# Optimization experiments

Measured on AMD Instinct MI355X. Metric: run time of the kernel, lower is better.

## Reference

```python
import jax, jax.numpy as jnp
import numpy as np

N = 8192      # points
NOBJ = 8      # objects
H = 64        # hidden_size (required by channel arithmetic, see notes)
CDIM = 128
K = 20
KNN = 360
EPS = 1e-5


def _lrelu(x):
    return jnp.where(x >= 0, x, 0.2 * x)


def _inorm2d(x):  # x: [C, N, K]; InstanceNorm2d, affine=False, biased var
    m = x.mean(axis=(1, 2), keepdims=True)
    v = ((x - m) ** 2).mean(axis=(1, 2), keepdims=True)
    return (x - m) / jnp.sqrt(v + EPS)


def _inorm1d(x):  # x: [C, L]
    m = x.mean(axis=1, keepdims=True)
    v = ((x - m) ** 2).mean(axis=1, keepdims=True)
    return (x - m) / jnp.sqrt(v + EPS)


def _block2d(W, f):  # 1x1 conv (no bias) + InstanceNorm2d + LeakyReLU(0.2)
    return _lrelu(_inorm2d(jnp.einsum('oc,cnk->onk', W, f)))


def _block1d(W, f):
    return _lrelu(_inorm1d(W @ f))


def _edge_feat(xc, idx):  # xc: [C, N], idx: [N, k] -> [2C, N, k]
    xt = xc.T                                   # [N, C]
    nb = xt[idx]                                # [N, k, C] gather
    ctr = jnp.broadcast_to(xt[:, None, :], nb.shape)
    return jnp.concatenate([nb - ctr, ctr], axis=2).transpose(2, 0, 1)


def _knn_idx(x, tag, k):  # kNN within same node_tag, self excluded
    xs = jax.lax.stop_gradient(x)
    sq = jnp.sum(xs * xs, axis=1)
    d2 = sq[:, None] + sq[None, :] - 2.0 * (xs @ xs.T)
    valid = (tag[:, None] == tag[None, :]) & ~jnp.eye(xs.shape[0], dtype=bool)
    d2 = jnp.where(valid, d2, jnp.inf)
    _, idx = jax.lax.top_k(-d2, k)              # ascending distance order
    return idx


def setup_inputs() -> dict:
    key = jax.random.key(0)
    ks = jax.random.split(key, 16)
    x = jax.random.normal(ks[0], (N, 3), dtype=jnp.float32)
    node_tag = (jnp.arange(N, dtype=jnp.int32) // (N // NOBJ))  # equal groups

    def w(k, o, i):
        return jax.random.normal(k, (o, i), dtype=jnp.float32) * (1.0 / np.sqrt(i))

    return {
        'x': x, 'node_tag': node_tag, 'n_obj': NOBJ,
        'W1': w(ks[1], H, 6),       'W2': w(ks[2], H, H),
        'W3': w(ks[3], H, 2 * H),   'W4': w(ks[4], H, H),
        'W5': w(ks[5], H, 2 * H),   'W6': w(ks[6], H, H),
        'W7': w(ks[7], H, 2 * H),   'W8': w(ks[8], H, H),
        'W9': w(ks[9], 128, 4 * H),
        'W10': w(ks[10], 2 * H, 3 * H),
        'W11': w(ks[11], 2 * H, 3 * H),
        'W12': w(ks[12], H, 3 * H),
        'W13': w(ks[13], H, 2 * H),
        'Wr': w(ks[14], CDIM, H),
    }


def reference(x, node_tag, n_obj, W1, W2, W3, W4, W5, W6, W7, W8, W9, W10,
              W11, W12, W13, Wr):
    n = x.shape[0]
    idx = _knn_idx(x, node_tag, KNN)            # [N, 360]

    f = _edge_feat(x.T, idx[:, :K])             # [6, N, 20]
    x1 = _block2d(W2, _block2d(W1, f)).max(axis=-1)            # [H, N]
    f = _edge_feat(x1, idx[:, :40:2])
    x2 = _block2d(W4, _block2d(W3, f)).max(axis=-1) + x1
    f = _edge_feat(x2, idx[:, :120:6])
    x3 = _block2d(W6, _block2d(W5, f)).max(axis=-1) + x2
    f = _edge_feat(x3, idx[:, :360:18])
    x4 = _block2d(W8, _block2d(W7, f)).max(axis=-1) + x3

    g = _block1d(W9, jnp.concatenate([x1, x2, x3, x4], axis=0))  # [128, N]
    g = jnp.broadcast_to(g.max(axis=1, keepdims=True), (128, n))

    x4 = _block1d(W10, jnp.concatenate([g, x4], axis=0))   # [2H, N]
    x3 = _block1d(W11, jnp.concatenate([x4, x3], axis=0))  # [2H, N]
    x2 = _block1d(W12, jnp.concatenate([x3, x2], axis=0))  # [H, N]
    x1 = _block1d(W13, jnp.concatenate([x2, x1], axis=0))  # [H, N]

    code = (Wr @ x1).T                                     # [N, c_dim]
    tag = node_tag.astype(jnp.int32)
    sums = jax.ops.segment_sum(code, tag, num_segments=n_obj)
    cnt = jax.ops.segment_sum(jnp.ones((n,), code.dtype), tag,
                              num_segments=n_obj)
    return sums / jnp.maximum(cnt, 1.0)[:, None]           # [n_obj, c_dim]
```

## Files before the change

### kernel.cpp

```cpp
#include <hip/hip_runtime.h>
#include <hip/hip_bf16.h>
#include <stdint.h>

typedef __hip_bfloat16 bf16;

#define NPTS 8192
#define KSEL 20
#define MBIG (NPTS*KSEL)
#define EPSN 1e-5f

__device__ __forceinline__ float lrelu(float x){ return x >= 0.f ? x : 0.2f*x; }
__device__ __forceinline__ float ldx(const void* p, int i, int isbf){
  return isbf ? __bfloat162float(((const bf16*)p)[i]) : ((const float*)p)[i];
}
__device__ __forceinline__ unsigned fenc(float x){
  unsigned u = __float_as_uint(x);
  return (u & 0x80000000u) ? ~u : (u | 0x80000000u);
}
__device__ __forceinline__ float fdec(unsigned u){
  return __uint_as_float((u & 0x80000000u) ? (u & 0x7FFFFFFFu) : ~u);
}
__device__ __forceinline__ unsigned long long u64min(unsigned long long a, unsigned long long b){ return a<b?a:b; }
__device__ __forceinline__ unsigned long long u64max(unsigned long long a, unsigned long long b){ return a<b?b:a; }
__device__ __forceinline__ void ce(unsigned long long &a, unsigned long long &b, bool asc){
  unsigned long long mn = a<b?a:b, mx = a<b?b:a;
  a = asc ? mn : mx;
  b = asc ? mx : mn;
}

__global__ void zero_kernel(float* __restrict__ p, int n){
  int i = blockIdx.x*256 + threadIdx.x;
  if (i < n) p[i] = 0.f;
}

__global__ void detect_kernel(const void* __restrict__ x, int* __restrict__ badf){
  int i = blockIdx.x*256 + threadIdx.x;
  int bad = 0;
  for (; i < NPTS*3; i += gridDim.x*256){
    float v = __bfloat162float(((const bf16*)x)[i]);
    if (!(fabsf(v) < 1000.0f)) bad = 1;
  }
  if (__any(bad) && (threadIdx.x & 63) == 0) atomicOr(badf, 1);
}

__global__ __launch_bounds__(256) void knn_kernel(const void* __restrict__ x,
                                                  const int* __restrict__ tag,
                                                  int* __restrict__ idxc,
                                                  const int* __restrict__ flagp){
  __shared__ unsigned long long keysL[1024];
  const int isbf = (*flagp == 0);
  const int i = blockIdx.x;
  const int base = (i >> 10) << 10;
  const int t = threadIdx.x;
  const float xi = ldx(x, i*3+0, isbf);
  const float yi = ldx(x, i*3+1, isbf);
  const float zi = ldx(x, i*3+2, isbf);
  const float sqi = xi*xi + yi*yi + zi*zi;
  const int tagi = tag[i];

  unsigned long long v[4];
  #pragma unroll
  for (int r = 0; r < 4; r++){
    int j = 4*t + r, gj = base + j;
    float xj = ldx(x, gj*3+0, isbf);
    float yj = ldx(x, gj*3+1, isbf);
    float zj = ldx(x, gj*3+2, isbf);
    float sqj = xj*xj + yj*yj + zj*zj;
    float dot = xi*xj + yi*yj + zi*zj;
    float d2 = sqi + sqj - 2.0f*dot;
    bool valid = (gj != i) && (tag[gj] == tagi);
    unsigned k = valid ? fenc(d2) : 0xFFFFFFFFu;
    v[r] = ((unsigned long long)k << 32) | (unsigned)gj;
  }

  #pragma unroll
  for (int ksz = 2; ksz <= 1024; ksz <<= 1){
    #pragma unroll
    for (int jj = ksz >> 1; jj > 0; jj >>= 1){
      if (jj >= 256){
        __syncthreads();
        keysL[4*t+0] = v[0]; keysL[4*t+1] = v[1];
        keysL[4*t+2] = v[2]; keysL[4*t+3] = v[3];
        __syncthreads();
        const int pt = t ^ (jj >> 2);
        const bool keep_min = (((t & (ksz >> 2)) == 0) == ((t & (jj >> 2)) == 0));
        #pragma unroll
        for (int r = 0; r < 4; r++){
          unsigned long long o = keysL[4*pt + r];
          v[r] = keep_min ? u64min(v[r], o) : u64max(v[r], o);
        }
      } else if (jj >= 4){
        const int mask = jj >> 2;
        const bool keep_min = (((t & (ksz >> 2)) == 0) == ((t & mask) == 0));
        #pragma unroll
        for (int r = 0; r < 4; r++){
          unsigned long long o = __shfl_xor(v[r], mask, 64);
          v[r] = keep_min ? u64min(v[r], o) : u64max(v[r], o);
        }
      } else if (jj == 2){
        const bool asc = ((t & (ksz >> 2)) == 0);
        ce(v[0], v[2], asc);
        ce(v[1], v[3], asc);
      } else {
        if (ksz == 2){
          ce(v[0], v[1], true);
          ce(v[2], v[3], false);
        } else {
          const bool asc = ((t & (ksz >> 2)) == 0);
          ce(v[0], v[1], asc);
          ce(v[2], v[3], asc);
        }
      }
    }
  }

  __syncthreads();
  keysL[4*t+0] = v[0]; keysL[4*t+1] = v[1];
  keysL[4*t+2] = v[2]; keysL[4*t+3] = v[3];
  __syncthreads();
  if (t < 80){
    int s = t / 20, k = t - s*20;
    int step = (s == 0) ? 1 : (s == 1) ? 2 : (s == 2) ? 6 : 18;
    idxc[i*80 + t] = (int)(keysL[k*step] & 0xFFFFFFFFu);
  }
}

template<int KIN>
__global__ __launch_bounds__(256) void pq_kernel(
    const void* __restrict__ xin, const float* __restrict__ prev,
    const void* __restrict__ Wc, float* __restrict__ Pt, float* __restrict__ Qt,
    const int* __restrict__ flagp)
{
  __shared__ float WaS[16][KIN];
  __shared__ float WdS[16][KIN];
  const int isbf = (*flagp == 0);
  const int t = threadIdx.x;
  const int n0 = (blockIdx.x & 31) * 256;
  const int cg = (blockIdx.x >> 5) * 16;
  for (int l = t; l < 16*KIN; l += 256){
    int r = l / KIN, k = l - r*KIN;
    float wa = ldx(Wc, (cg + r)*(2*KIN) + k, isbf);
    float wb = ldx(Wc, (cg + r)*(2*KIN) + KIN + k, isbf);
    WaS[r][k] = wa;
    WdS[r][k] = wb - wa;
  }
  __syncthreads();
  const int n = n0 + t;
  float xr[KIN];
  if (KIN == 3){
    #pragma unroll
    for (int k = 0; k < KIN; k++) xr[k] = ldx(xin, n*3 + k, isbf);
  } else {
    #pragma unroll 8
    for (int k = 0; k < KIN; k++) xr[k] = prev[k*NPTS + n];
  }
  float pv[16], qv[16];
  #pragma unroll
  for (int r = 0; r < 16; r++){
    float p = 0.f, q = 0.f;
    #pragma unroll 8
    for (int k = 0; k < KIN; k++){
      p += WaS[r][k] * xr[k];
      q += WdS[r][k] * xr[k];
    }
    pv[r] = p; qv[r] = q;
  }
  #pragma unroll
  for (int r4 = 0; r4 < 4; r4++){
    *(float4*)&Pt[n*64 + cg + r4*4] = make_float4(pv[r4*4], pv[r4*4+1], pv[r4*4+2], pv[r4*4+3]);
    *(float4*)&Qt[n*64 + cg + r4*4] = make_float4(qv[r4*4], qv[r4*4+1], qv[r4*4+2], qv[r4*4+3]);
  }
}

__global__ __launch_bounds__(256) void stats1_kernel(
    const float* __restrict__ Pt, const float* __restrict__ Qt,
    const int* __restrict__ idxc, int sidx, float* __restrict__ stats)
{
  __shared__ float Qs[1024];
  __shared__ int ids[320];
  const int t = threadIdx.x;
  const int n0 = blockIdx.x * 16;
  for (int l = t; l < 1024; l += 256) Qs[l] = Qt[n0*64 + l];
  for (int l = t; l < 320; l += 256){
    int p = l / 20, k = l - p*20;
    ids[l] = idxc[(n0+p)*80 + sidx*20 + k] & (NPTS-1);
  }
  __syncthreads();
  const int tx = t & 15, ty = t >> 4;
  const int kq = tx >> 2, p0 = (tx & 3)*4;
  float sacc[4] = {0,0,0,0}, qacc[4] = {0,0,0,0};
  #pragma unroll
  for (int s = 0; s < 5; s++){
    int k = s*4 + kq;
    #pragma unroll
    for (int j = 0; j < 4; j++){
      int p = p0 + j;
      int nb = ids[p*20 + k];
      float4 pvv = *(const float4*)&Pt[nb*64 + ty*4];
      float4 qvv = *(const float4*)&Qs[p*64 + ty*4];
      float e0 = pvv.x+qvv.x, e1 = pvv.y+qvv.y, e2 = pvv.z+qvv.z, e3 = pvv.w+qvv.w;
      sacc[0]+=e0; sacc[1]+=e1; sacc[2]+=e2; sacc[3]+=e3;
      qacc[0]+=e0*e0; qacc[1]+=e1*e1; qacc[2]+=e2*e2; qacc[3]+=e3*e3;
    }
  }
  #pragma unroll
  for (int i = 0; i < 4; i++){
    float s = sacc[i], q = qacc[i];
    #pragma unroll
    for (int off = 8; off; off >>= 1){
      s += __shfl_down(s, off, 16);
      q += __shfl_down(q, off, 16);
    }
    if (tx == 0){
      atomicAdd(&stats[ty*4+i], s);
      atomicAdd(&stats[256+ty*4+i], q);
    }
  }
}

__global__ __launch_bounds__(256) void conv2_kernel(
    const float* __restrict__ Pt, const float* __restrict__ Qt,
    const int* __restrict__ idxc, int sidx,
    const void* __restrict__ W2c,
    const float* __restrict__ st1raw,
    float* __restrict__ stats2,
    float* __restrict__ rawmax,
    const int* __restrict__ flagp)
{
  __shared__ __align__(16) float G[64][64];
  __shared__ __align__(16) float Wt2[64][64];
  __shared__ float Qs[1024];
  __shared__ int ids[320];
  __shared__ float nm1[64], niv1[64];
  const int isbf = (*flagp == 0);
  const int t = threadIdx.x;
  const int n0 = blockIdx.x * 16;
  const float invMB = 1.0f/(float)MBIG;
  for (int l = t; l < 4096; l += 256){
    int r = l & 63, k = l >> 6;
    Wt2[k][r] = ldx(W2c, r*64 + k, isbf);
  }
  for (int l = t; l < 1024; l += 256) Qs[l] = Qt[n0*64 + l];
  for (int l = t; l < 320; l += 256){
    int p = l / 20, k = l - p*20;
    ids[l] = idxc[(n0+p)*80 + sidx*20 + k] & (NPTS-1);
  }
  if (t < 64){
    float m = st1raw[t] * invMB;
    float v = st1raw[256+t]*invMB - m*m;
    nm1[t] = m;
    niv1[t] = 1.0f / sqrtf(fmaxf(v, 0.f) + EPSN);
  }
  __syncthreads();

  const int tx = t & 15, ty = t >> 4;
  const int kq = tx >> 2, p0 = (tx & 3)*4;
  float sacc[4] = {0,0,0,0}, qacc[4] = {0,0,0,0};
  float mx[4][4];
  #pragma unroll
  for (int i = 0; i < 4; i++)
    #pragma unroll
    for (int j = 0; j < 4; j++) mx[i][j] = -3.4e38f;

  for (int s = 0; s < 5; s++){
    int k = s*4 + kq;
    #pragma unroll
    for (int j = 0; j < 4; j++){
      int p = p0 + j;
      int nb = ids[p*20 + k];
      float4 pvv = *(const float4*)&Pt[nb*64 + ty*4];
      float4 qvv = *(const float4*)&Qs[p*64 + ty*4];
      float e[4] = {pvv.x+qvv.x, pvv.y+qvv.y, pvv.z+qvv.z, pvv.w+qvv.w};
      #pragma unroll
      for (int i = 0; i < 4; i++){
        int r = ty*4 + i;
        G[r][tx*4 + j] = lrelu((e[i] - nm1[r]) * niv1[r]);
      }
    }
    __syncthreads();
    float acc[4][4] = {{0.f}};
    #pragma unroll 4
    for (int k2 = 0; k2 < 64; k2++){
      float4 a = *(const float4*)&Wt2[k2][ty*4];
      float4 b = *(const float4*)&G[k2][tx*4];
      acc[0][0]+=a.x*b.x; acc[0][1]+=a.x*b.y; acc[0][2]+=a.x*b.z; acc[0][3]+=a.x*b.w;
      acc[1][0]+=a.y*b.x; acc[1][1]+=a.y*b.y; acc[1][2]+=a.y*b.z; acc[1][3]+=a.y*b.w;
      acc[2][0]+=a.z*b.x; acc[2][1]+=a.z*b.y; acc[2][2]+=a.z*b.z; acc[2][3]+=a.z*b.w;
      acc[3][0]+=a.w*b.x; acc[3][1]+=a.w*b.y; acc[3][2]+=a.w*b.z; acc[3][3]+=a.w*b.w;
    }
    #pragma unroll
    for (int i = 0; i < 4; i++)
      #pragma unroll
      for (int j = 0; j < 4; j++){
        float v = acc[i][j];
        sacc[i] += v;
        qacc[i] += v*v;
        mx[i][j] = fmaxf(mx[i][j], v);
      }
    __syncthreads();
  }

  #pragma unroll
  for (int i = 0; i < 4; i++){
    float s = sacc[i], q = qacc[i];
    #pragma unroll
    for (int off = 8; off; off >>= 1){
      s += __shfl_down(s, off, 16);
      q += __shfl_down(q, off, 16);
    }
    if (tx == 0){
      atomicAdd(&stats2[ty*4+i], s);
      atomicAdd(&stats2[256+ty*4+i], q);
    }
  }
  #pragma unroll
  for (int i = 0; i < 4; i++)
    #pragma unroll
    for (int j = 0; j < 4; j++){
      mx[i][j] = fmaxf(mx[i][j], __shfl_xor(mx[i][j], 4, 16));
      mx[i][j] = fmaxf(mx[i][j], __shfl_xor(mx[i][j], 8, 16));
    }
  if (tx < 4){
    #pragma unroll
    for (int i = 0; i < 4; i++){
      int c = ty*4 + i;
      #pragma unroll
      for (int j = 0; j < 4; j++){
        int n = n0 + tx*4 + j;
        rawmax[c*NPTS + n] = mx[i][j];
      }
    }
  }
}

__global__ __launch_bounds__(256) void maxres_kernel(
    const float* __restrict__ rawmax, const float* __restrict__ st2raw,
    const float* __restrict__ resid, float* __restrict__ xout)
{
  const float invMB = 1.0f/(float)MBIG;
  int g = blockIdx.x*256 + threadIdx.x;
  int c = g >> 13;
  float m = st2raw[c] * invMB;
  float v = st2raw[256+c]*invMB - m*m;
  float iv = 1.0f / sqrtf(fmaxf(v, 0.f) + EPSN);
  float y = lrelu((rawmax[g] - m) * iv);
  xout[g] = y + (resid ? resid[g] : 0.f);
}

__global__ __launch_bounds__(256) void gemm1d_kernel(
    const void* __restrict__ W, int ldw, int koffW,
    const float* __restrict__ A, const float* __restrict__ Araw, float invA, int CA,
    const float* __restrict__ B, int CB,
    const float* __restrict__ cvec,
    float* __restrict__ Y,
    float* __restrict__ stats, unsigned* __restrict__ maxenc,
    const int* __restrict__ flagp)
{
  __shared__ __align__(16) float Fs[64][64];
  __shared__ __align__(16) float Wt[64][64];
  __shared__ float am[128], aiv[128];
  const int t = threadIdx.x;
  const int isbf = (*flagp == 0);
  const int colbase = (blockIdx.x & 127) * 64;
  const int rb = (blockIdx.x >> 7) * 64;
  const int tx = t & 15, ty = t >> 4;
  if (Araw && t < CA){
    float m = Araw[t] * invA;
    float v = Araw[256+t]*invA - m*m;
    am[t] = m;
    aiv[t] = 1.0f / sqrtf(fmaxf(v, 0.f) + EPSN);
  }
  float acc[4][4] = {{0.f}};
  const int CTOT = CA + CB;
  for (int kc = 0; kc < CTOT; kc += 64){
    for (int l = t; l < 64*64; l += 256){
      int r = l & 63, kk = l >> 6;
      Wt[kk][r] = ldx(W, (rb + r)*ldw + koffW + kc + kk, isbf);
    }
    __syncthreads();
    for (int l = t; l < 64*64; l += 256){
      int kk = l >> 6, j = l & 63;
      int k = kc + kk;
      float v;
      if (k < CA){
        v = A[k*NPTS + colbase + j];
        if (Araw) v = lrelu((v - am[k]) * aiv[k]);
      } else {
        v = B[(k - CA)*NPTS + colbase + j];
      }
      Fs[kk][j] = v;
    }
    __syncthreads();
    #pragma unroll 4
    for (int kk = 0; kk < 64; kk++){
      float4 a = *(const float4*)&Wt[kk][ty*4];
      float4 b = *(const float4*)&Fs[kk][tx*4];
      acc[0][0]+=a.x*b.x; acc[0][1]+=a.x*b.y; acc[0][2]+=a.x*b.z; acc[0][3]+=a.x*b.w;
      acc[1][0]+=a.y*b.x; acc[1][1]+=a.y*b.y; acc[1][2]+=a.y*b.z; acc[1][3]+=a.y*b.w;
      acc[2][0]+=a.z*b.x; acc[2][1]+=a.z*b.y; acc[2][2]+=a.z*b.z; acc[2][3]+=a.z*b.w;
      acc[3][0]+=a.w*b.x; acc[3][1]+=a.w*b.y; acc[3][2]+=a.w*b.z; acc[3][3]+=a.w*b.w;
    }
    __syncthreads();
  }
  #pragma unroll
  for (int rr = 0; rr < 4; rr++){
    int r = rb + ty*4 + rr;
    float cv = cvec ? cvec[r] : 0.f;
    float4 v = make_float4(acc[rr][0]+cv, acc[rr][1]+cv, acc[rr][2]+cv, acc[rr][3]+cv);
    float sum = v.x + v.y + v.z + v.w;
    float q = v.x*v.x + v.y*v.y + v.z*v.z + v.w*v.w;
    float mxv = fmaxf(fmaxf(v.x, v.y), fmaxf(v.z, v.w));
    #pragma unroll
    for (int off = 8; off; off >>= 1){
      sum += __shfl_down(sum, off, 16);
      q   += __shfl_down(q, off, 16);
      mxv  = fmaxf(mxv, __shfl_down(mxv, off, 16));
    }
    if (tx == 0){
      atomicAdd(&stats[r], sum);
      atomicAdd(&stats[256 + r], q);
      if (maxenc) atomicMax(&maxenc[r], fenc(mxv));
    }
    if (Y) *(float4*)&Y[r*NPTS + colbase + tx*4] = v;
  }
}

__global__ void finalize_g_kernel(float* __restrict__ statsG,
    unsigned* __restrict__ gmaxenc, float* __restrict__ c0,
    const void* __restrict__ W10, const int* __restrict__ flagp)
{
  __shared__ float gsh[128];
  const int isbf = (*flagp == 0);
  int c = threadIdx.x;
  if (c < 128){
    float m = statsG[c] * (1.f/NPTS);
    float v = statsG[256+c]*(1.f/NPTS) - m*m;
    float iv = 1.0f / sqrtf(fmaxf(v, 0.f) + EPSN);
    gsh[c] = lrelu((fdec(gmaxenc[c]) - m) * iv);
  }
  __syncthreads();
  if (c < 128){
    float s = 0.f;
    for (int j = 0; j < 128; j++) s += ldx(W10, c*192 + j, isbf) * gsh[j];
    c0[c] = s;
  }
}

__global__ __launch_bounds__(256) void segsum_kernel(
    const float* __restrict__ ybuf, const float* __restrict__ straw,
    const int* __restrict__ tag, float* __restrict__ seg, float* __restrict__ cnt)
{
  const float invMN = 1.0f/(float)NPTS;
  int g = blockIdx.x*256 + threadIdx.x;
  int c = g >> 13, n = g & (NPTS-1);
  float m = straw[c] * invMN;
  float vv = straw[256+c]*invMN - m*m;
  float iv = 1.0f / sqrtf(fmaxf(vv, 0.f) + EPSN);
  float v = lrelu((ybuf[c*NPTS + n] - m) * iv);
  int tg = tag[n] & 7;
  int lane = threadIdx.x & 63;
  int t0 = __shfl(tg, 0, 64);
  bool uni = __all(tg == t0);
  if (uni){
    #pragma unroll
    for (int off = 32; off; off >>= 1) v += __shfl_down(v, off, 64);
    if (lane == 0){
      atomicAdd(&seg[t0*64 + c], v);
      if (c == 0) atomicAdd(cnt + t0, 64.f);
    }
  } else {
    atomicAdd(&seg[tg*64 + c], v);
    if (c == 0) atomicAdd(cnt + tg, 1.f);
  }
}

__global__ void final_kernel(const void* __restrict__ Wr,
    const float* __restrict__ seg, const float* __restrict__ cnt,
    void* __restrict__ out, int total, const int* __restrict__ flagp)
{
  const int isbf = (*flagp == 0);
  int q = blockIdx.x*blockDim.x + threadIdx.x;
  if (q >= total) return;
  int g = q >> 7, c = q & 127;
  float s = 0.f;
  for (int j = 0; j < 64; j++) s += ldx(Wr, c*64 + j, isbf) * seg[g*64 + j];
  float r = s / fmaxf(cnt[g], 1.f);
  if (isbf) ((bf16*)out)[q] = __float2bfloat16(r);
  else      ((float*)out)[q] = r;
}

extern "C" void kernel_launch(void* const* d_in, const int* in_sizes, int n_in,
                              void* d_out, int out_size, void* d_ws, size_t ws_size,
                              hipStream_t stream)
{
  const void* x   = d_in[0];
  const int* tag  = (const int*)d_in[1];
  const void* W1  = d_in[3];
  const void* W2  = d_in[4];
  const void* W3  = d_in[5];
  const void* W4  = d_in[6];
  const void* W5  = d_in[7];
  const void* W6  = d_in[8];
  const void* W7  = d_in[9];
  const void* W8  = d_in[10];
  const void* W9  = d_in[11];
  const void* W10 = d_in[12];
  const void* W11 = d_in[13];
  const void* W12 = d_in[14];
  const void* W13 = d_in[15];
  const void* Wr  = d_in[16];

  char* ws = (char*)d_ws;
  int*      idxc = (int*)ws;
  float*    xs   = (float*)(ws + 2621440);
  float* x1 = xs;
  float* x2 = xs +  64*NPTS;
  float* x3 = xs + 128*NPTS;
  float* x4 = xs + 192*NPTS;
  float*    y0   = (float*)(ws + 11010048);
  float*    y1   = (float*)(ws + 15204352);
  float*    rmax = (float*)(ws + 19398656);
  float*    Pt   = y0;
  float*    Qt   = y0 + 64*NPTS;
  float*    st   = (float*)(ws + 21495808);
  auto L = [&](int l){ return st + l*1024; };
  int*      flag     = (int*)(st + 13312);
  unsigned* gmaxenc  = (unsigned*)(st + 13440);
  float*    c0v      = st + 13568;
  float*    seg      = st + 13824;
  float*    cnt      = seg + 512;

  zero_kernel<<<64, 256, 0, stream>>>(st, 16384);
  detect_kernel<<<12, 256, 0, stream>>>(x, flag);
  knn_kernel<<<NPTS, 256, 0, stream>>>(x, tag, idxc, flag);

#define STAGE(KINV, XIN, PREV, WA, WB, LA, LB, XOUT, RES, SIDX)                              \
  pq_kernel<KINV><<<128, 256, 0, stream>>>(XIN, PREV, WA, Pt, Qt, flag);                     \
  stats1_kernel<<<512, 256, 0, stream>>>(Pt, Qt, idxc, SIDX, LA);                            \
  conv2_kernel<<<512, 256, 0, stream>>>(Pt, Qt, idxc, SIDX, WB, LA, LB, rmax, flag);         \
  maxres_kernel<<<64*NPTS/256, 256, 0, stream>>>(rmax, LB, RES, XOUT);

  STAGE(3,  x,       nullptr, W1, W2, L(0), L(1), x1, nullptr, 0)
  STAGE(64, nullptr, x1,      W3, W4, L(2), L(3), x2, x1,      1)
  STAGE(64, nullptr, x2,      W5, W6, L(4), L(5), x3, x2,      2)
  STAGE(64, nullptr, x3,      W7, W8, L(6), L(7), x4, x3,      3)
#undef STAGE

  gemm1d_kernel<<<256, 256, 0, stream>>>(W9, 256, 0, xs, nullptr, 0.f, 256,
                                         nullptr, 0, nullptr, nullptr, L(8), gmaxenc, flag);
  finalize_g_kernel<<<1, 128, 0, stream>>>(L(8), gmaxenc, c0v, W10, flag);

  const float invMN = 1.0f/(float)NPTS;
  gemm1d_kernel<<<256, 256, 0, stream>>>(W10, 192, 128, nullptr, nullptr, 0.f, 0,
                                         x4, 64, c0v, y0, L(9), nullptr, flag);
  gemm1d_kernel<<<256, 256, 0, stream>>>(W11, 192, 0, y0, L(9), invMN, 128,
                                         x3, 64, nullptr, y1, L(10), nullptr, flag);
  gemm1d_kernel<<<128, 256, 0, stream>>>(W12, 192, 0, y1, L(10), invMN, 128,
                                         x2, 64, nullptr, y0, L(11), nullptr, flag);
  gemm1d_kernel<<<128, 256, 0, stream>>>(W13, 128, 0, y0, L(11), invMN, 64,
                                         x1, 64, nullptr, y1, L(12), nullptr, flag);

  segsum_kernel<<<64*NPTS/256, 256, 0, stream>>>(y1, L(12), tag, seg, cnt);
  final_kernel<<<4, 256, 0, stream>>>(Wr, seg, cnt, d_out, out_size, flag);
}
```

Before: 1.040 ms.

## Use bf16 MFMA for conv2 and 1D GEMM kernels with register-held weights

Replaces the scalar FP32 shared-memory GEMMs in conv2_kernel and gemm1d_kernel with bf16 16x16x32 MFMA instructions. Weight fragments are now loaded straight into registers instead of being staged through shared memory, and activations are packed to bf16 in a padded shared tile. gemm1d becomes templated on the total input channels so the A-fragment array size is fixed at compile time. This targets the FP32 FMA cost of these matmuls, at the price of lower precision from bf16 rounding of the activations and weights.

```diff
diff --git a/kernel.cpp b/kernel.cpp
--- a/kernel.cpp
+++ b/kernel.cpp
@@ -3,6 +3,9 @@
 #include <stdint.h>
 
 typedef __hip_bfloat16 bf16;
+typedef __attribute__((ext_vector_type(8))) short bfrag;
+typedef __attribute__((ext_vector_type(4))) short s16x4;
+typedef __attribute__((ext_vector_type(4))) float f32x4;
 
 #define NPTS 8192
 #define KSEL 20
@@ -12,6 +15,14 @@
 __device__ __forceinline__ float lrelu(float x){ return x >= 0.f ? x : 0.2f*x; }
 __device__ __forceinline__ float ldx(const void* p, int i, int isbf){
   return isbf ? __bfloat162float(((const bf16*)p)[i]) : ((const float*)p)[i];
+}
+__device__ __forceinline__ short f2bs(float f){
+  union { bf16 h; short s; } u;
+  u.h = __float2bfloat16(f);
+  return u.s;
+}
+__device__ __forceinline__ f32x4 mfma16(bfrag a, bfrag b, f32x4 c){
+  return __builtin_amdgcn_mfma_f32_16x16x32_bf16(a, b, c, 0, 0, 0);
 }
 __device__ __forceinline__ unsigned fenc(float x){
   unsigned u = __float_as_uint(x);
@@ -176,7 +187,7 @@
     const float* __restrict__ Pt, const float* __restrict__ Qt,
     const int* __restrict__ idxc, int sidx, float* __restrict__ stats)
 {
-  __shared__ float Qs[1024];
+  __shared__ __align__(16) float Qs[1024];
   __shared__ int ids[320];
   const int t = threadIdx.x;
   const int n0 = blockIdx.x * 16;
@@ -227,19 +238,15 @@
     float* __restrict__ rawmax,
     const int* __restrict__ flagp)
 {
-  __shared__ __align__(16) float G[64][64];
-  __shared__ __align__(16) float Wt2[64][64];
-  __shared__ float Qs[1024];
+  __shared__ __align__(16) short Gs[64][72];
+  __shared__ __align__(16) float Qs[1024];
   __shared__ int ids[320];
   __shared__ float nm1[64], niv1[64];
   const int isbf = (*flagp == 0);
   const int t = threadIdx.x;
   const int n0 = blockIdx.x * 16;
   const float invMB = 1.0f/(float)MBIG;
-  for (int l = t; l < 4096; l += 256){
-    int r = l & 63, k = l >> 6;
-    Wt2[k][r] = ldx(W2c, r*64 + k, isbf);
-  }
+
   for (int l = t; l < 1024; l += 256) Qs[l] = Qt[n0*64 + l];
   for (int l = t; l < 320; l += 256){
     int p = l / 20, k = l - p*20;
@@ -251,85 +258,68 @@
     nm1[t] = m;
     niv1[t] = 1.0f / sqrtf(fmaxf(v, 0.f) + EPSN);
   }
+
+  const int lane = t & 63, w = t >> 6;
+  const int nn = lane & 15, quad = lane >> 4;
+  bfrag af0, af1;
+  #pragma unroll
+  for (int j = 0; j < 8; j++){
+    af0[j] = f2bs(ldx(W2c, (16*w + nn)*64 +      quad*8 + j, isbf));
+    af1[j] = f2bs(ldx(W2c, (16*w + nn)*64 + 32 + quad*8 + j, isbf));
+  }
   __syncthreads();
 
   const int tx = t & 15, ty = t >> 4;
-  const int kq = tx >> 2, p0 = (tx & 3)*4;
   float sacc[4] = {0,0,0,0}, qacc[4] = {0,0,0,0};
-  float mx[4][4];
-  #pragma unroll
-  for (int i = 0; i < 4; i++)
-    #pragma unroll
-    for (int j = 0; j < 4; j++) mx[i][j] = -3.4e38f;
+  float mxr[4] = {-3.4e38f,-3.4e38f,-3.4e38f,-3.4e38f};
 
   for (int s = 0; s < 5; s++){
-    int k = s*4 + kq;
     #pragma unroll
     for (int j = 0; j < 4; j++){
-      int p = p0 + j;
-      int nb = ids[p*20 + k];
+      int cg = tx*4 + j;
+      int q = cg >> 4, p = cg & 15;
+      int nb = ids[p*20 + s*4 + q];
       float4 pvv = *(const float4*)&Pt[nb*64 + ty*4];
       float4 qvv = *(const float4*)&Qs[p*64 + ty*4];
-      float e[4] = {pvv.x+qvv.x, pvv.y+qvv.y, pvv.z+qvv.z, pvv.w+qvv.w};
+      s16x4 gv;
+      gv[0] = f2bs(lrelu((pvv.x+qvv.x - nm1[ty*4+0]) * niv1[ty*4+0]));
+      gv[1] = f2bs(lrelu((pvv.y+qvv.y - nm1[ty*4+1]) * niv1[ty*4+1]));
+      gv[2] = f2bs(lrelu((pvv.z+qvv.z - nm1[ty*4+2]) * niv1[ty*4+2]));
+      gv[3] = f2bs(lrelu((pvv.w+qvv.w - nm1[ty*4+3]) * niv1[ty*4+3]));
+      *(s16x4*)&Gs[cg][ty*4] = gv;
+    }
+    __syncthreads();
+    #pragma unroll
+    for (int q = 0; q < 4; q++){
+      bfrag b0 = *(bfrag*)&Gs[q*16 + nn][quad*8];
+      bfrag b1 = *(bfrag*)&Gs[q*16 + nn][32 + quad*8];
+      f32x4 acc = {0.f, 0.f, 0.f, 0.f};
+      acc = mfma16(af0, b0, acc);
+      acc = mfma16(af1, b1, acc);
       #pragma unroll
-      for (int i = 0; i < 4; i++){
-        int r = ty*4 + i;
-        G[r][tx*4 + j] = lrelu((e[i] - nm1[r]) * niv1[r]);
+      for (int r = 0; r < 4; r++){
+        float v = acc[r];
+        sacc[r] += v; qacc[r] += v*v;
+        mxr[r] = fmaxf(mxr[r], v);
       }
     }
     __syncthreads();
-    float acc[4][4] = {{0.f}};
-    #pragma unroll 4
-    for (int k2 = 0; k2 < 64; k2++){
-      float4 a = *(const float4*)&Wt2[k2][ty*4];
-      float4 b = *(const float4*)&G[k2][tx*4];
-      acc[0][0]+=a.x*b.x; acc[0][1]+=a.x*b.y; acc[0][2]+=a.x*b.z; acc[0][3]+=a.x*b.w;
-      acc[1][0]+=a.y*b.x; acc[1][1]+=a.y*b.y; acc[1][2]+=a.y*b.z; acc[1][3]+=a.y*b.w;
-      acc[2][0]+=a.z*b.x; acc[2][1]+=a.z*b.y; acc[2][2]+=a.z*b.z; acc[2][3]+=a.z*b.w;
-      acc[3][0]+=a.w*b.x; acc[3][1]+=a.w*b.y; acc[3][2]+=a.w*b.z; acc[3][3]+=a.w*b.w;
-    }
-    #pragma unroll
-    for (int i = 0; i < 4; i++)
-      #pragma unroll
-      for (int j = 0; j < 4; j++){
-        float v = acc[i][j];
-        sacc[i] += v;
-        qacc[i] += v*v;
-        mx[i][j] = fmaxf(mx[i][j], v);
-      }
-    __syncthreads();
-  }
-
-  #pragma unroll
-  for (int i = 0; i < 4; i++){
-    float s = sacc[i], q = qacc[i];
+  }
+
+  #pragma unroll
+  for (int r = 0; r < 4; r++){
+    int rr = 16*w + quad*4 + r;
+    float s = sacc[r], q2 = qacc[r];
     #pragma unroll
     for (int off = 8; off; off >>= 1){
-      s += __shfl_down(s, off, 16);
-      q += __shfl_down(q, off, 16);
-    }
-    if (tx == 0){
-      atomicAdd(&stats2[ty*4+i], s);
-      atomicAdd(&stats2[256+ty*4+i], q);
-    }
-  }
-  #pragma unroll
-  for (int i = 0; i < 4; i++)
-    #pragma unroll
-    for (int j = 0; j < 4; j++){
-      mx[i][j] = fmaxf(mx[i][j], __shfl_xor(mx[i][j], 4, 16));
-      mx[i][j] = fmaxf(mx[i][j], __shfl_xor(mx[i][j], 8, 16));
-    }
-  if (tx < 4){
-    #pragma unroll
-    for (int i = 0; i < 4; i++){
-      int c = ty*4 + i;
-      #pragma unroll
-      for (int j = 0; j < 4; j++){
-        int n = n0 + tx*4 + j;
-        rawmax[c*NPTS + n] = mx[i][j];
-      }
-    }
+      s  += __shfl_down(s, off, 16);
+      q2 += __shfl_down(q2, off, 16);
+    }
+    if (nn == 0){
+      atomicAdd(&stats2[rr], s);
+      atomicAdd(&stats2[256+rr], q2);
+    }
+    rawmax[rr*NPTS + n0 + nn] = mxr[r];
   }
 }
 
@@ -347,81 +337,96 @@
   xout[g] = y + (resid ? resid[g] : 0.f);
 }
 
+template<int CTOT>
 __global__ __launch_bounds__(256) void gemm1d_kernel(
     const void* __restrict__ W, int ldw, int koffW,
     const float* __restrict__ A, const float* __restrict__ Araw, float invA, int CA,
-    const float* __restrict__ B, int CB,
+    const float* __restrict__ B,
     const float* __restrict__ cvec,
     float* __restrict__ Y,
     float* __restrict__ stats, unsigned* __restrict__ maxenc,
     const int* __restrict__ flagp)
 {
-  __shared__ __align__(16) float Fs[64][64];
-  __shared__ __align__(16) float Wt[64][64];
-  __shared__ float am[128], aiv[128];
+  __shared__ __align__(16) short Fs[64][72];
+  __shared__ float am[256], aiv[256];
   const int t = threadIdx.x;
   const int isbf = (*flagp == 0);
   const int colbase = (blockIdx.x & 127) * 64;
   const int rb = (blockIdx.x >> 7) * 64;
-  const int tx = t & 15, ty = t >> 4;
+  const int lane = t & 63, w = t >> 6;
+  const int nn = lane & 15, quad = lane >> 4;
+
   if (Araw && t < CA){
-    float m = Araw[t] * invA;
+    float m = Araw[t]*invA;
     float v = Araw[256+t]*invA - m*m;
-    am[t] = m;
-    aiv[t] = 1.0f / sqrtf(fmaxf(v, 0.f) + EPSN);
-  }
-  float acc[4][4] = {{0.f}};
-  const int CTOT = CA + CB;
+    am[t] = m; aiv[t] = 1.0f/sqrtf(fmaxf(v,0.f)+EPSN);
+  }
+
+  constexpr int K32 = CTOT >> 5;
+  bfrag af[K32];
+  const int arow = rb + 16*w + nn;
+  #pragma unroll
+  for (int f = 0; f < K32; f++)
+    #pragma unroll
+    for (int j = 0; j < 8; j++)
+      af[f][j] = f2bs(ldx(W, arow*ldw + koffW + f*32 + quad*8 + j, isbf));
+
+  f32x4 acc[4] = {};
+  const int jcol = t & 63, kg = t >> 6;
+
   for (int kc = 0; kc < CTOT; kc += 64){
-    for (int l = t; l < 64*64; l += 256){
-      int r = l & 63, kk = l >> 6;
-      Wt[kk][r] = ldx(W, (rb + r)*ldw + koffW + kc + kk, isbf);
-    }
     __syncthreads();
-    for (int l = t; l < 64*64; l += 256){
-      int kk = l >> 6, j = l & 63;
-      int k = kc + kk;
-      float v;
-      if (k < CA){
-        v = A[k*NPTS + colbase + j];
-        if (Araw) v = lrelu((v - am[k]) * aiv[k]);
-      } else {
-        v = B[(k - CA)*NPTS + colbase + j];
+    #pragma unroll
+    for (int u = 0; u < 4; u++){
+      int kl = kg*16 + u*4;
+      s16x4 pk;
+      #pragma unroll
+      for (int z = 0; z < 4; z++){
+        int k = kc + kl + z;
+        float v;
+        if (k < CA){
+          v = A[k*NPTS + colbase + jcol];
+          if (Araw) v = lrelu((v - am[k]) * aiv[k]);
+        } else {
+          v = B[(k-CA)*NPTS + colbase + jcol];
+        }
+        pk[z] = f2bs(v);
       }
-      Fs[kk][j] = v;
+      *(s16x4*)&Fs[jcol][kl] = pk;
     }
     __syncthreads();
-    #pragma unroll 4
-    for (int kk = 0; kk < 64; kk++){
-      float4 a = *(const float4*)&Wt[kk][ty*4];
-      float4 b = *(const float4*)&Fs[kk][tx*4];
-      acc[0][0]+=a.x*b.x; acc[0][1]+=a.x*b.y; acc[0][2]+=a.x*b.z; acc[0][3]+=a.x*b.w;
-      acc[1][0]+=a.y*b.x; acc[1][1]+=a.y*b.y; acc[1][2]+=a.y*b.z; acc[1][3]+=a.y*b.w;
-      acc[2][0]+=a.z*b.x; acc[2][1]+=a.z*b.y; acc[2][2]+=a.z*b.z; acc[2][3]+=a.z*b.w;
-      acc[3][0]+=a.w*b.x; acc[3][1]+=a.w*b.y; acc[3][2]+=a.w*b.z; acc[3][3]+=a.w*b.w;
-    }
-    __syncthreads();
-  }
-  #pragma unroll
-  for (int rr = 0; rr < 4; rr++){
-    int r = rb + ty*4 + rr;
-    float cv = cvec ? cvec[r] : 0.f;
-    float4 v = make_float4(acc[rr][0]+cv, acc[rr][1]+cv, acc[rr][2]+cv, acc[rr][3]+cv);
-    float sum = v.x + v.y + v.z + v.w;
-    float q = v.x*v.x + v.y*v.y + v.z*v.z + v.w*v.w;
-    float mxv = fmaxf(fmaxf(v.x, v.y), fmaxf(v.z, v.w));
+    const int f0 = kc >> 5;
+    #pragma unroll
+    for (int q = 0; q < 4; q++){
+      bfrag b0 = *(bfrag*)&Fs[q*16+nn][quad*8];
+      bfrag b1 = *(bfrag*)&Fs[q*16+nn][32 + quad*8];
+      acc[q] = mfma16(af[f0],   b0, acc[q]);
+      acc[q] = mfma16(af[f0+1], b1, acc[q]);
+    }
+  }
+
+  #pragma unroll
+  for (int r = 0; r < 4; r++){
+    int rr = rb + 16*w + quad*4 + r;
+    float cv = cvec ? cvec[rr] : 0.f;
+    float sum = 0.f, q2 = 0.f, mxv = -3.4e38f;
+    #pragma unroll
+    for (int q = 0; q < 4; q++){
+      float v = acc[q][r] + cv;
+      sum += v; q2 += v*v; mxv = fmaxf(mxv, v);
+      if (Y) Y[rr*NPTS + colbase + q*16 + nn] = v;
+    }
     #pragma unroll
     for (int off = 8; off; off >>= 1){
       sum += __shfl_down(sum, off, 16);
-      q   += __shfl_down(q, off, 16);
+      q2  += __shfl_down(q2, off, 16);
       mxv  = fmaxf(mxv, __shfl_down(mxv, off, 16));
     }
-    if (tx == 0){
-      atomicAdd(&stats[r], sum);
-      atomicAdd(&stats[256 + r], q);
-      if (maxenc) atomicMax(&maxenc[r], fenc(mxv));
-    }
-    if (Y) *(float4*)&Y[r*NPTS + colbase + tx*4] = v;
+    if (nn == 0){
+      atomicAdd(&stats[rr], sum);
+      atomicAdd(&stats[256+rr], q2);
+      if (maxenc) atomicMax(&maxenc[rr], fenc(mxv));
+    }
   }
 }
 
@@ -546,19 +551,19 @@
   STAGE(64, nullptr, x3,      W7, W8, L(6), L(7), x4, x3,      3)
 #undef STAGE
 
-  gemm1d_kernel<<<256, 256, 0, stream>>>(W9, 256, 0, xs, nullptr, 0.f, 256,
-                                         nullptr, 0, nullptr, nullptr, L(8), gmaxenc, flag);
+  gemm1d_kernel<256><<<256, 256, 0, stream>>>(W9, 256, 0, xs, nullptr, 0.f, 256,
+                                              nullptr, nullptr, nullptr, L(8), gmaxenc, flag);
   finalize_g_kernel<<<1, 128, 0, stream>>>(L(8), gmaxenc, c0v, W10, flag);
 
   const float invMN = 1.0f/(float)NPTS;
-  gemm1d_kernel<<<256, 256, 0, stream>>>(W10, 192, 128, nullptr, nullptr, 0.f, 0,
-                                         x4, 64, c0v, y0, L(9), nullptr, flag);
-  gemm1d_kernel<<<256, 256, 0, stream>>>(W11, 192, 0, y0, L(9), invMN, 128,
-                                         x3, 64, nullptr, y1, L(10), nullptr, flag);
-  gemm1d_kernel<<<128, 256, 0, stream>>>(W12, 192, 0, y1, L(10), invMN, 128,
-                                         x2, 64, nullptr, y0, L(11), nullptr, flag);
-  gemm1d_kernel<<<128, 256, 0, stream>>>(W13, 128, 0, y0, L(11), invMN, 64,
-                                         x1, 64, nullptr, y1, L(12), nullptr, flag);
+  gemm1d_kernel<64> <<<256, 256, 0, stream>>>(W10, 192, 128, nullptr, nullptr, 0.f, 0,
+                                              x4, c0v, y0, L(9), nullptr, flag);
+  gemm1d_kernel<192><<<256, 256, 0, stream>>>(W11, 192, 0, y0, L(9), invMN, 128,
+                                              x3, nullptr, y1, L(10), nullptr, flag);
+  gemm1d_kernel<192><<<128, 256, 0, stream>>>(W12, 192, 0, y1, L(10), invMN, 128,
+                                              x2, nullptr, y0, L(11), nullptr, flag);
+  gemm1d_kernel<128><<<128, 256, 0, stream>>>(W13, 128, 0, y0, L(11), invMN, 64,
+                                              x1, nullptr, y1, L(12), nullptr, flag);
 
   segsum_kernel<<<64*NPTS/256, 256, 0, stream>>>(y1, L(12), tag, seg, cnt);
   final_kernel<<<4, 256, 0, stream>>>(Wr, seg, cnt, d_out, out_size, flag);
```

Result: faster. 981.7 us (-5.6%).
